# Optimization experiments

Measured on AMD Instinct MI355X. Metric: run time of the kernel, lower is better.

The kernel has to match this reference:

```python
import jax, jax.numpy as jnp
import numpy as np

NUM_GRAPHS = 256  # fixed number of segments (batch.max()+1 in the torch code)

def setup_inputs() -> dict:
    key = jax.random.key(0)
    k1, k2, k3, k4, k5 = jax.random.split(key, 5)
    N, D, H = 200000, 256, 128
    x = jax.random.normal(k1, (N, D), dtype=jnp.float32)
    batch = jnp.sort(jax.random.randint(k2, (N,), 0, NUM_GRAPHS)).astype(jnp.int64)
    # attention MLP params: Linear(D->H), Tanh, Linear(H->1)
    w1 = jax.random.normal(k3, (D, H), dtype=jnp.float32) / np.sqrt(D)
    b1 = jnp.zeros((H,), dtype=jnp.float32)
    w2 = jax.random.normal(k4, (H, 1), dtype=jnp.float32) / np.sqrt(H)
    b2 = jnp.zeros((1,), dtype=jnp.float32)
    return {"x": x, "batch": batch, "w1": w1, "b1": b1, "w2": w2, "b2": b2}

def reference(x, batch, w1, b1, w2, b2):
    # attention scores: Linear -> tanh -> Linear -> [N,1]
    scores = jnp.tanh(x @ w1 + b1) @ w2 + b2          # [N,1]
    # NOTE: faithful to the original: softmax over ALL nodes (dim=0), not per-graph
    attn = jax.nn.softmax(scores, axis=0)              # [N,1]
    weighted = x * attn                                # [N,D]
    # masked per-graph sum == segment sum over graph ids
    out = jax.ops.segment_sum(weighted, batch, num_segments=NUM_GRAPHS)  # [B,D]
    return out
```

## Files before the change

### kernel.cpp

```cpp
#include <hip/hip_runtime.h>

#define NGRAPHS 256
#define DIM     256
#define HID     128
#define TILE    128

typedef __attribute__((ext_vector_type(8))) short bf16x8;
typedef __attribute__((ext_vector_type(4))) float f32x4;

__device__ __forceinline__ ushort f2bf_rne(float f) {
    unsigned u = __float_as_uint(f);
    unsigned r = u + 0x7fffu + ((u >> 16) & 1u);
    return (ushort)(r >> 16);
}
__device__ __forceinline__ float tanh_fast(float x) {
    float e = __expf(2.0f * x);
    return 1.0f - 2.0f * __builtin_amdgcn_rcpf(1.0f + e);
}

__device__ __forceinline__ void glds16(const void* g, void* l) {
    __builtin_amdgcn_global_load_lds(
        (const __attribute__((address_space(1))) unsigned int*)g,
        (__attribute__((address_space(3))) unsigned int*)l, 16, 0, 0);
}

__device__ __forceinline__ void cvt8(float4 v0, float4 v1, bf16x8& h, bf16x8& l) {
    float f[8] = {v0.x, v0.y, v0.z, v0.w, v1.x, v1.y, v1.z, v1.w};
    unsigned hu[8], lu[8];
#pragma unroll
    for (int i = 0; i < 8; ++i) {
        unsigned u = __float_as_uint(f[i]);
        unsigned hb = u & 0xffff0000u;
        hu[i] = u;
        lu[i] = __float_as_uint(f[i] - __uint_as_float(hb));
    }
    union { unsigned w[4]; bf16x8 v; } H, L;
#pragma unroll
    for (int j = 0; j < 4; ++j) {
        H.w[j] = (hu[2 * j] >> 16) | (hu[2 * j + 1] & 0xffff0000u);
        L.w[j] = (lu[2 * j] >> 16) | (lu[2 * j + 1] & 0xffff0000u);
    }
    h = H.v; l = L.v;
}

__global__ void k_prep(const float* __restrict__ w1, ushort* __restrict__ w1f)
{
    int idx = blockIdx.x * 256 + threadIdx.x;
    int k  = idx >> 7, nn = idx & 127;
    int ks = k >> 5, lhi = (k >> 3) & 3, j = k & 7;
    int nf = nn >> 4, llo = nn & 15;
    int lane = lhi * 16 + llo;
    w1f[(ks * 8 + nf) * 512 + lane * 8 + j] = f2bf_rne(w1[idx]);
}

__global__ __launch_bounds__(256, 2) void k_scores(
    const float* __restrict__ x, const int* __restrict__ batch,
    const ushort* __restrict__ w1f,
    const float* __restrict__ b1, const float* __restrict__ w2,
    const float* __restrict__ b2,
    float* __restrict__ wsp, float* __restrict__ wse, int* __restrict__ wsid,
    int n)
{
    __shared__ __align__(16) unsigned char smem[3 * 24576];
    __shared__ float evals[TILE];
    __shared__ int   gid[TILE];
    __shared__ float ep[4];
    float (*sred)[2][DIM] = (float(*)[2][DIM])smem;

    const int t    = threadIdx.x;
    const int b    = blockIdx.x;
    const int r0   = b * TILE;
    const int wid  = t >> 6;
    const int lane = t & 63;
    const int lhi  = lane >> 4;
    const int llo  = lane & 15;

    if (t < TILE) {
        int r = r0 + t;
        gid[t] = batch[r < n ? r : (n - 1)];
    }

    size_t xoff[4];
    int    xl[4];
#pragma unroll
    for (int i = 0; i < 4; ++i) {
        int p = i * 256 + t;
        int r = p >> 3, s = p & 7;
        int q = s ^ (r & 7);
        int rsrc = r0 + r; if (rsrc >= n) rsrc = n - 1;
        xoff[i] = (size_t)rsrc * DIM + q * 4;
        xl[i]   = (i * 256 + wid * 64) * 16;
    }
    size_t boff[2];
    int    bl[2];
#pragma unroll
    for (int i = 0; i < 2; ++i) {
        boff[i] = (size_t)(i * 256 + t) * 8;
        bl[i]   = (i * 256 + wid * 64) * 16;
    }

#define XBUF(sel) ((float*)(smem + (sel) * 24576))
#define BBUF(sel) ((ushort*)(smem + (sel) * 24576 + 16384))
#define STAGE(sel, KS) do {                                              \
    _Pragma("unroll")                                                    \
    for (int i = 0; i < 4; ++i)                                          \
        glds16(x + xoff[i] + (KS) * 32, smem + (sel) * 24576 + xl[i]);   \
    _Pragma("unroll")                                                    \
    for (int i = 0; i < 2; ++i)                                          \
        glds16(w1f + (size_t)(KS) * 4096 + boff[i],                      \
               smem + (sel) * 24576 + 16384 + bl[i]);                    \
} while (0)

    f32x4 acc[2][8];
#pragma unroll
    for (int i = 0; i < 2; ++i)
#pragma unroll
        for (int j = 0; j < 8; ++j) acc[i][j] = (f32x4){0.f, 0.f, 0.f, 0.f};

    const int ra0 = wid * 32 + llo;
    const int ra1 = ra0 + 16;
    const int rb7 = ra0 & 7;
    const int c00 = (ra0 * 8 + ((2 * lhi)     ^ rb7)) * 4;
    const int c01 = (ra0 * 8 + ((2 * lhi + 1) ^ rb7)) * 4;
    const int c10 = (ra1 * 8 + ((2 * lhi)     ^ rb7)) * 4;
    const int c11 = (ra1 * 8 + ((2 * lhi + 1) ^ rb7)) * 4;

    STAGE(0, 0);
    STAGE(1, 1);
#pragma unroll
    for (int ks = 0; ks < 8; ++ks) {
        const int cur = ks % 3;
        if (ks < 7) {
            asm volatile("s_waitcnt vmcnt(6)" ::: "memory");
        } else {
            asm volatile("s_waitcnt vmcnt(0)" ::: "memory");
        }
        __builtin_amdgcn_sched_barrier(0);
        __builtin_amdgcn_s_barrier();
        __builtin_amdgcn_sched_barrier(0);
        if (ks < 6) STAGE((ks + 2) % 3, ks + 2);

        const float*  xsc = XBUF(cur);
        const ushort* bsc = BBUF(cur);
        float4 a0 = *(const float4*)&xsc[c00];
        float4 a1 = *(const float4*)&xsc[c01];
        float4 c0 = *(const float4*)&xsc[c10];
        float4 c1 = *(const float4*)&xsc[c11];
        bf16x8 ah0, al0, ah1, al1;
        cvt8(a0, a1, ah0, al0);
        cvt8(c0, c1, ah1, al1);

#pragma unroll
        for (int nf = 0; nf < 8; ++nf) {
            bf16x8 bh = *(const bf16x8*)&bsc[nf * 512 + lane * 8];
            acc[0][nf] = __builtin_amdgcn_mfma_f32_16x16x32_bf16(ah0, bh, acc[0][nf], 0, 0, 0);
            acc[1][nf] = __builtin_amdgcn_mfma_f32_16x16x32_bf16(ah1, bh, acc[1][nf], 0, 0, 0);
            acc[0][nf] = __builtin_amdgcn_mfma_f32_16x16x32_bf16(al0, bh, acc[0][nf], 0, 0, 0);
            acc[1][nf] = __builtin_amdgcn_mfma_f32_16x16x32_bf16(al1, bh, acc[1][nf], 0, 0, 0);
        }
    }
#undef STAGE
#undef XBUF
#undef BBUF

    float b2v = b2[0];
    float b1v[8], w2v[8];
#pragma unroll
    for (int nf = 0; nf < 8; ++nf) {
        b1v[nf] = b1[nf * 16 + llo];
        w2v[nf] = w2[nf * 16 + llo];
    }
    float sc[8];
#pragma unroll
    for (int mf = 0; mf < 2; ++mf)
#pragma unroll
        for (int rg = 0; rg < 4; ++rg) {
            float p = 0.f;
#pragma unroll
            for (int nf = 0; nf < 8; ++nf)
                p += tanh_fast(acc[mf][nf][rg] + b1v[nf]) * w2v[nf];
            sc[mf * 4 + rg] = p;
        }
#pragma unroll
    for (int off = 1; off < 16; off <<= 1)
#pragma unroll
        for (int q = 0; q < 8; ++q) sc[q] += __shfl_xor(sc[q], off, 64);

    if (llo == 0) {
#pragma unroll
        for (int mf = 0; mf < 2; ++mf)
#pragma unroll
            for (int rg = 0; rg < 4; ++rg) {
                int row = wid * 32 + mf * 16 + lhi * 4 + rg;
                float s = sc[mf * 4 + rg] + b2v;
                evals[row] = (r0 + row < n) ? __expf(s) : 0.f;
            }
    }
    __syncthreads();

    {
        const int g0 = gid[0];
        float4 a0 = {0.f, 0.f, 0.f, 0.f}, a1 = {0.f, 0.f, 0.f, 0.f};
        for (int bt = 0; bt < 4; ++bt) {
            float4 xv[8];
#pragma unroll
            for (int j = 0; j < 8; ++j) {
                int rsrc = r0 + wid * 32 + bt * 8 + j;
                if (rsrc >= n) rsrc = n - 1;
                xv[j] = *(const float4*)(x + (size_t)rsrc * DIM + lane * 4);
            }
#pragma unroll
            for (int j = 0; j < 8; ++j) {
                int row = wid * 32 + bt * 8 + j;
                float e = evals[row];
                if (gid[row] != g0) {
                    a1.x = fmaf(e, xv[j].x, a1.x); a1.y = fmaf(e, xv[j].y, a1.y);
                    a1.z = fmaf(e, xv[j].z, a1.z); a1.w = fmaf(e, xv[j].w, a1.w);
                } else {
                    a0.x = fmaf(e, xv[j].x, a0.x); a0.y = fmaf(e, xv[j].y, a0.y);
                    a0.z = fmaf(e, xv[j].z, a0.z); a0.w = fmaf(e, xv[j].w, a0.w);
                }
            }
        }
        *(float4*)&sred[wid][0][lane * 4] = a0;
        *(float4*)&sred[wid][1][lane * 4] = a1;
    }
    __syncthreads();
    {
        float s0 = sred[0][0][t] + sred[1][0][t] + sred[2][0][t] + sred[3][0][t];
        float s1 = sred[0][1][t] + sred[1][1][t] + sred[2][1][t] + sred[3][1][t];
        wsp[(size_t)b * 512 + t]       = s0;
        wsp[(size_t)b * 512 + 256 + t] = s1;
        if (t == 0) wsid[b] = gid[0];
    }

    float rsum = (t < TILE) ? evals[t] : 0.f;
#pragma unroll
    for (int off = 32; off; off >>= 1) rsum += __shfl_down(rsum, off, 64);
    if ((t & 63) == 0) ep[t >> 6] = rsum;
    __syncthreads();
    if (t == 0) wse[b] = ep[0] + ep[1];
}

__global__ __launch_bounds__(256) void k_combine(
    const int* __restrict__ batch, const float* __restrict__ wsp,
    const float* __restrict__ wse, const int* __restrict__ wsid,
    float* __restrict__ out, int n, int nblk)
{
    __shared__ float sred[256];
    __shared__ int bounds[2];
    const int g = blockIdx.x;
    const int d = threadIdx.x;

    float p = 0.f;
    for (int i = d; i < nblk; i += 256) p += wse[i];
    sred[d] = p;
    __syncthreads();
    for (int s = 128; s; s >>= 1) {
        if (d < s) sred[d] += sred[d + s];
        __syncthreads();
    }
    const float S = sred[0];

    if (d < 2) {
        int v = g + d;
        int lo = 0, hi = n;
        while (lo < hi) { int mid = (lo + hi) >> 1; if (batch[mid] < v) lo = mid + 1; else hi = mid; }
        bounds[d] = lo;
    }
    __syncthreads();

    const int st = bounds[0], en = bounds[1];
    float acc = 0.f;
    if (st < en) {
        for (int bb = st >> 7; bb <= (en - 1) >> 7; ++bb) {
            int slot = (wsid[bb] == g) ? 0 : 1;
            acc += wsp[(size_t)bb * 512 + slot * 256 + d];
        }
    }
    out[g * 256 + d] = acc / S;
}

extern "C" void kernel_launch(void* const* d_in, const int* in_sizes, int n_in,
                              void* d_out, int out_size, void* d_ws, size_t ws_size,
                              hipStream_t stream)
{
    const float* x     = (const float*)d_in[0];
    const int*   batch = (const int*)d_in[1];
    const float* w1    = (const float*)d_in[2];
    const float* b1    = (const float*)d_in[3];
    const float* w2    = (const float*)d_in[4];
    const float* b2    = (const float*)d_in[5];
    float* out = (float*)d_out;

    const int n    = in_sizes[1];
    const int nblk = (n + TILE - 1) / TILE;

    ushort* w1f = (ushort*)d_ws;
    float*  wsp = (float*)((char*)d_ws + (size_t)DIM * HID * sizeof(ushort));
    float*  wse = wsp + (size_t)nblk * 512;
    int*    wsid = (int*)(wse + nblk);

    k_prep<<<dim3(DIM * HID / 256), dim3(256), 0, stream>>>(w1, w1f);
    k_scores<<<dim3(nblk), dim3(256), 0, stream>>>(x, batch, w1f,
                                                   b1, w2, b2, wsp, wse, wsid, n);
    k_combine<<<dim3(NGRAPHS), dim3(256), 0, stream>>>(batch, wsp, wse, wsid,
                                                       out, n, nblk);
}
```

Before: 88.58 us.

## Drop split-bf16 low part and stage x through registers as bf16

Removes the hi/lo bf16 split of x, so the score GEMM uses a single bf16 MFMA pass instead of two, halving matrix work. x is now loaded into registers, rounded to bf16 and written to a padded LDS layout. LDS is cut so launch bounds can allow 3 blocks per CU. The staging schedule is restructured with triple-buffered x and double-buffered w1, plus explicit waitcnts. This loses precision in the attention scores, which feed a softmax over all nodes, and the pipeline now has more register pressure.

```diff
diff --git a/kernel.cpp b/kernel.cpp
--- a/kernel.cpp
+++ b/kernel.cpp
@@ -17,30 +17,16 @@
     float e = __expf(2.0f * x);
     return 1.0f - 2.0f * __builtin_amdgcn_rcpf(1.0f + e);
 }
-
+__device__ __forceinline__ unsigned pack2(float a, float b) {
+    unsigned ua = __float_as_uint(a), ub = __float_as_uint(b);
+    unsigned ra = ua + 0x7fffu + ((ua >> 16) & 1u);
+    unsigned rb = ub + 0x7fffu + ((ub >> 16) & 1u);
+    return (ra >> 16) | (rb & 0xffff0000u);
+}
 __device__ __forceinline__ void glds16(const void* g, void* l) {
     __builtin_amdgcn_global_load_lds(
         (const __attribute__((address_space(1))) unsigned int*)g,
         (__attribute__((address_space(3))) unsigned int*)l, 16, 0, 0);
-}
-
-__device__ __forceinline__ void cvt8(float4 v0, float4 v1, bf16x8& h, bf16x8& l) {
-    float f[8] = {v0.x, v0.y, v0.z, v0.w, v1.x, v1.y, v1.z, v1.w};
-    unsigned hu[8], lu[8];
-#pragma unroll
-    for (int i = 0; i < 8; ++i) {
-        unsigned u = __float_as_uint(f[i]);
-        unsigned hb = u & 0xffff0000u;
-        hu[i] = u;
-        lu[i] = __float_as_uint(f[i] - __uint_as_float(hb));
-    }
-    union { unsigned w[4]; bf16x8 v; } H, L;
-#pragma unroll
-    for (int j = 0; j < 4; ++j) {
-        H.w[j] = (hu[2 * j] >> 16) | (hu[2 * j + 1] & 0xffff0000u);
-        L.w[j] = (lu[2 * j] >> 16) | (lu[2 * j + 1] & 0xffff0000u);
-    }
-    h = H.v; l = L.v;
 }
 
 __global__ void k_prep(const float* __restrict__ w1, ushort* __restrict__ w1f)
@@ -53,7 +39,7 @@
     w1f[(ks * 8 + nf) * 512 + lane * 8 + j] = f2bf_rne(w1[idx]);
 }
 
-__global__ __launch_bounds__(256, 2) void k_scores(
+__global__ __launch_bounds__(256, 3) void k_scores(
     const float* __restrict__ x, const int* __restrict__ batch,
     const ushort* __restrict__ w1f,
     const float* __restrict__ b1, const float* __restrict__ w2,
@@ -61,7 +47,7 @@
     float* __restrict__ wsp, float* __restrict__ wse, int* __restrict__ wsid,
     int n)
 {
-    __shared__ __align__(16) unsigned char smem[3 * 24576];
+    __shared__ __align__(16) unsigned char smem[47104];
     __shared__ float evals[TILE];
     __shared__ int   gid[TILE];
     __shared__ float ep[4];
@@ -80,36 +66,42 @@
         gid[t] = batch[r < n ? r : (n - 1)];
     }
 
-    size_t xoff[4];
-    int    xl[4];
-#pragma unroll
-    for (int i = 0; i < 4; ++i) {
-        int p = i * 256 + t;
-        int r = p >> 3, s = p & 7;
-        int q = s ^ (r & 7);
-        int rsrc = r0 + r; if (rsrc >= n) rsrc = n - 1;
-        xoff[i] = (size_t)rsrc * DIM + q * 4;
-        xl[i]   = (i * 256 + wid * 64) * 16;
-    }
-    size_t boff[2];
-    int    bl[2];
+    int xrow = r0 + (t >> 1); if (xrow >= n) xrow = n - 1;
+    const float* xp = x + (size_t)xrow * DIM + (t & 1) * 16;
+    const int    wb = (t >> 1) * 80 + (t & 1) * 32;
+
+    size_t boff[2]; int bl[2];
 #pragma unroll
     for (int i = 0; i < 2; ++i) {
         boff[i] = (size_t)(i * 256 + t) * 8;
         bl[i]   = (i * 256 + wid * 64) * 16;
     }
 
-#define XBUF(sel) ((float*)(smem + (sel) * 24576))
-#define BBUF(sel) ((ushort*)(smem + (sel) * 24576 + 16384))
-#define STAGE(sel, KS) do {                                              \
-    _Pragma("unroll")                                                    \
-    for (int i = 0; i < 4; ++i)                                          \
-        glds16(x + xoff[i] + (KS) * 32, smem + (sel) * 24576 + xl[i]);   \
-    _Pragma("unroll")                                                    \
-    for (int i = 0; i < 2; ++i)                                          \
-        glds16(w1f + (size_t)(KS) * 4096 + boff[i],                      \
-               smem + (sel) * 24576 + 16384 + bl[i]);                    \
+#define XBUF(s3) (smem + (s3) * 10240)
+#define BBUF(s2) (smem + 30720 + (s2) * 8192)
+#define STAGE_B(s2, KS) do {                                         \
+    glds16(w1f + (size_t)(KS) * 4096 + boff[0], BBUF(s2) + bl[0]);   \
+    glds16(w1f + (size_t)(KS) * 4096 + boff[1], BBUF(s2) + bl[1]);   \
 } while (0)
+#define XLOAD(st, KS) do {                                           \
+    xr[st][0] = *(const float4*)(xp + (KS) * 32);                    \
+    xr[st][1] = *(const float4*)(xp + (KS) * 32 + 4);                \
+    xr[st][2] = *(const float4*)(xp + (KS) * 32 + 8);                \
+    xr[st][3] = *(const float4*)(xp + (KS) * 32 + 12);               \
+} while (0)
+#define CVT_WRITE(st, s3) do {                                       \
+    uint4 w0, w1v;                                                   \
+    w0.x  = pack2(xr[st][0].x, xr[st][0].y);                         \
+    w0.y  = pack2(xr[st][0].z, xr[st][0].w);                         \
+    w0.z  = pack2(xr[st][1].x, xr[st][1].y);                         \
+    w0.w  = pack2(xr[st][1].z, xr[st][1].w);                         \
+    w1v.x = pack2(xr[st][2].x, xr[st][2].y);                         \
+    w1v.y = pack2(xr[st][2].z, xr[st][2].w);                         \
+    w1v.z = pack2(xr[st][3].x, xr[st][3].y);                         \
+    w1v.w = pack2(xr[st][3].z, xr[st][3].w);                         \
+    *(uint4*)(XBUF(s3) + wb)      = w0;                              \
+    *(uint4*)(XBUF(s3) + wb + 16) = w1v;                             \
+} while (0)
 
     f32x4 acc[2][8];
 #pragma unroll
@@ -117,49 +109,55 @@
 #pragma unroll
         for (int j = 0; j < 8; ++j) acc[i][j] = (f32x4){0.f, 0.f, 0.f, 0.f};
 
-    const int ra0 = wid * 32 + llo;
-    const int ra1 = ra0 + 16;
-    const int rb7 = ra0 & 7;
-    const int c00 = (ra0 * 8 + ((2 * lhi)     ^ rb7)) * 4;
-    const int c01 = (ra0 * 8 + ((2 * lhi + 1) ^ rb7)) * 4;
-    const int c10 = (ra1 * 8 + ((2 * lhi)     ^ rb7)) * 4;
-    const int c11 = (ra1 * 8 + ((2 * lhi + 1) ^ rb7)) * 4;
-
-    STAGE(0, 0);
-    STAGE(1, 1);
+    const int ra0    = wid * 32 + llo;
+    const int ra1    = ra0 + 16;
+    const int abase0 = ra0 * 80 + lhi * 16;
+    const int abase1 = ra1 * 80 + lhi * 16;
+
+    float4 xr[2][4];
+
+    XLOAD(0, 0);
+    __builtin_amdgcn_sched_barrier(0);
+    STAGE_B(0, 0);
+    __builtin_amdgcn_sched_barrier(0);
+    XLOAD(1, 1);
+    __builtin_amdgcn_sched_barrier(0);
+    asm volatile("s_waitcnt vmcnt(6)" ::: "memory");
+    __builtin_amdgcn_sched_barrier(0);
+    CVT_WRITE(0, 0);
+
 #pragma unroll
     for (int ks = 0; ks < 8; ++ks) {
-        const int cur = ks % 3;
-        if (ks < 7) {
-            asm volatile("s_waitcnt vmcnt(6)" ::: "memory");
-        } else {
-            asm volatile("s_waitcnt vmcnt(0)" ::: "memory");
-        }
+        if (ks < 7) asm volatile("s_waitcnt vmcnt(4) lgkmcnt(0)" ::: "memory");
+        else        asm volatile("s_waitcnt vmcnt(0) lgkmcnt(0)" ::: "memory");
         __builtin_amdgcn_sched_barrier(0);
         __builtin_amdgcn_s_barrier();
         __builtin_amdgcn_sched_barrier(0);
-        if (ks < 6) STAGE((ks + 2) % 3, ks + 2);
-
-        const float*  xsc = XBUF(cur);
-        const ushort* bsc = BBUF(cur);
-        float4 a0 = *(const float4*)&xsc[c00];
-        float4 a1 = *(const float4*)&xsc[c01];
-        float4 c0 = *(const float4*)&xsc[c10];
-        float4 c1 = *(const float4*)&xsc[c11];
-        bf16x8 ah0, al0, ah1, al1;
-        cvt8(a0, a1, ah0, al0);
-        cvt8(c0, c1, ah1, al1);
-
+
+        if (ks + 1 < 8) { STAGE_B((ks + 1) & 1, ks + 1); __builtin_amdgcn_sched_barrier(0); }
+        if (ks + 2 < 8) { XLOAD(ks & 1, ks + 2);         __builtin_amdgcn_sched_barrier(0); }
+
+        if (ks + 1 < 8) {
+            if (ks <= 5) asm volatile("s_waitcnt vmcnt(6)" ::: "memory");
+            else         asm volatile("s_waitcnt vmcnt(2)" ::: "memory");
+            __builtin_amdgcn_sched_barrier(0);
+            CVT_WRITE((ks + 1) & 1, (ks + 1) % 3);
+        }
+
+        const unsigned char* xb = XBUF(ks % 3);
+        const unsigned char* bb = BBUF(ks & 1);
+        bf16x8 ah0 = *(const bf16x8*)(xb + abase0);
+        bf16x8 ah1 = *(const bf16x8*)(xb + abase1);
 #pragma unroll
         for (int nf = 0; nf < 8; ++nf) {
-            bf16x8 bh = *(const bf16x8*)&bsc[nf * 512 + lane * 8];
+            bf16x8 bh = *(const bf16x8*)(bb + (nf * 512 + lane * 8) * 2);
             acc[0][nf] = __builtin_amdgcn_mfma_f32_16x16x32_bf16(ah0, bh, acc[0][nf], 0, 0, 0);
             acc[1][nf] = __builtin_amdgcn_mfma_f32_16x16x32_bf16(ah1, bh, acc[1][nf], 0, 0, 0);
-            acc[0][nf] = __builtin_amdgcn_mfma_f32_16x16x32_bf16(al0, bh, acc[0][nf], 0, 0, 0);
-            acc[1][nf] = __builtin_amdgcn_mfma_f32_16x16x32_bf16(al1, bh, acc[1][nf], 0, 0, 0);
-        }
-    }
-#undef STAGE
+        }
+    }
+#undef STAGE_B
+#undef XLOAD
+#undef CVT_WRITE
 #undef XBUF
 #undef BBUF
 
```

Result: no change. 87.22 us (-1.5%).
